# Performance work log

Hardware: AMD Instinct MI355X
Metric: run time of the kernel (lower is better)

The kernel has to match this reference:

```python
import jax, jax.numpy as jnp
import numpy as np

T, S, B, E, H = 1024, 1024, 4, 1024, 16
D = E // H
SCALE = D ** -0.5


def setup_inputs() -> dict:
    key = jax.random.key(0)
    ks = jax.random.split(key, 10)
    std = 0.02
    return {
        "q": jax.random.normal(ks[0], (T, B, E), jnp.float32),
        "k": jax.random.normal(ks[1], (S, B, E), jnp.float32),
        "v": jax.random.normal(ks[2], (S, B, E), jnp.float32),
        "Wq": jax.random.normal(ks[3], (E, E), jnp.float32) * std,
        "Wk": jax.random.normal(ks[4], (E, E), jnp.float32) * std,
        "Wv": jax.random.normal(ks[5], (E, E), jnp.float32) * std,
        "Wp": jax.random.normal(ks[6], (E, E), jnp.float32) * std,
        "bp": jnp.zeros((E,), jnp.float32),
        "attn_bias": jax.random.normal(ks[7], (B, H, T, S), jnp.float32) * std,
        "key_padding_mask": jax.random.bernoulli(ks[8], 0.1, (B, S)),
    }


def reference(q, k, v, Wq, Wk, Wv, Wp, bp, attn_bias, key_padding_mask):
    # projections (no bias: qkv_bias=False); torch Linear is x @ W.T
    qh = (q @ Wq.T).reshape(T, B, H, D).transpose(1, 2, 0, 3) * SCALE  # [B,H,T,D]
    kh = (k @ Wk.T).reshape(S, B, H, D).transpose(1, 2, 0, 3)          # [B,H,S,D]
    vh = (v @ Wv.T).reshape(S, B, H, D).transpose(1, 2, 0, 3)          # [B,H,S,D]

    scores = jnp.einsum("bhid,bhjd->bhij", qh, kh) + attn_bias        # [B,H,T,S]
    # detached max-subtract (as in original)
    scores = scores - jax.lax.stop_gradient(scores.max(axis=-1, keepdims=True))

    mask = key_padding_mask[:, None, None, :]                          # [B,1,1,S], True = masked
    neg = jnp.finfo(scores.dtype).min
    attn = jax.nn.softmax(jnp.where(mask, neg, scores), axis=-1)
    attn = jnp.where(mask, jnp.zeros((), scores.dtype), attn)          # XSoftmax: zero masked probs

    out = jnp.einsum("bhij,bhjd->bhid", attn, vh)                      # [B,H,T,D]
    out = out.transpose(2, 0, 1, 3).reshape(T, B, E)                   # [T,B,E]
    out = out @ Wp.T + bp                                              # output projection
    return (out, attn)
```

## Files before the change

kernel.cpp:

```cpp
#include <hip/hip_runtime.h>
#include <math.h>

constexpr int T_ = 1024, S_ = 1024, B_ = 4, E_ = 1024, H_ = 16, D_ = 64;
constexpr float SCALE_ = 0.125f;
constexpr size_t NH_ = (size_t)B_ * H_ * T_ * D_;
constexpr size_t EE_ = (size_t)E_ * E_;

typedef _Float16 h8 __attribute__((ext_vector_type(8)));
typedef _Float16 h4 __attribute__((ext_vector_type(4)));
typedef float f4 __attribute__((ext_vector_type(4)));

__device__ inline f4 mfma16(h8 a, h8 b, f4 c) {
    return __builtin_amdgcn_mfma_f32_16x16x32_f16(a, b, c, 0, 0, 0);
}

__global__ __launch_bounds__(256) void cvt_all(
    const float* __restrict__ q, const float* __restrict__ k,
    const float* __restrict__ v, const float* __restrict__ wq,
    const float* __restrict__ wk, const float* __restrict__ wv,
    const float* __restrict__ wp, _Float16* __restrict__ dst)
{
    const int i8 = blockIdx.x * 256 + threadIdx.x;
    constexpr int BIG = (int)(NH_ / 8);
    constexpr int WSZ = (int)(EE_ / 8);
    const float* src;
    int loc;
    if (i8 < 3 * BIG) {
        int t = i8 / BIG; loc = i8 - t * BIG;
        src = t == 0 ? q : (t == 1 ? k : v);
    } else {
        int r = i8 - 3 * BIG;
        int t = r / WSZ; loc = r - t * WSZ;
        src = t == 0 ? wq : (t == 1 ? wk : (t == 2 ? wv : wp));
    }
    const float* p = src + (size_t)loc * 8;
    float4 a = *(const float4*)p;
    float4 b = *(const float4*)(p + 4);
    h8 o;
    o[0] = (_Float16)a.x; o[1] = (_Float16)a.y;
    o[2] = (_Float16)a.z; o[3] = (_Float16)a.w;
    o[4] = (_Float16)b.x; o[5] = (_Float16)b.y;
    o[6] = (_Float16)b.z; o[7] = (_Float16)b.w;
    *(h8*)&dst[(size_t)i8 * 8] = o;
}

template <int MODE>
__global__ __launch_bounds__(512) void proj_gemm(
    const _Float16* __restrict__ A, const _Float16* __restrict__ W,
    const float* __restrict__ bias, void* __restrict__ Cv, float scale)
{
    __shared__ _Float16 As[128][72];
    __shared__ _Float16 Bs[128][72];

    const int m0 = blockIdx.x * 128, n0 = blockIdx.y * 128;
    const int tid = threadIdx.x;
    const int w = tid >> 6, l = tid & 63, lr = l & 15, lg = l >> 4;
    const int wr = w >> 2, wc = w & 3;

    f4 acc[4][2];
#pragma unroll
    for (int mi = 0; mi < 4; ++mi)
#pragma unroll
        for (int ni = 0; ni < 2; ++ni) acc[mi][ni] = (f4){0.f, 0.f, 0.f, 0.f};

    for (int k0 = 0; k0 < 1024; k0 += 64) {
#pragma unroll
        for (int i = 0; i < 2; ++i) {
            int f = tid + i * 512;
            int row = f >> 3, c = f & 7;
            *(h8*)&As[row][c * 8] = *(const h8*)&A[(size_t)(m0 + row) * 1024 + k0 + c * 8];
            *(h8*)&Bs[row][c * 8] = *(const h8*)&W[(size_t)(n0 + row) * 1024 + k0 + c * 8];
        }
        __syncthreads();
#pragma unroll
        for (int kk = 0; kk < 2; ++kk) {
            h8 af[4], bf[2];
#pragma unroll
            for (int mi = 0; mi < 4; ++mi)
                af[mi] = *(const h8*)&As[wr * 64 + mi * 16 + lr][kk * 32 + lg * 8];
#pragma unroll
            for (int ni = 0; ni < 2; ++ni)
                bf[ni] = *(const h8*)&Bs[wc * 32 + ni * 16 + lr][kk * 32 + lg * 8];
#pragma unroll
            for (int mi = 0; mi < 4; ++mi)
#pragma unroll
                for (int ni = 0; ni < 2; ++ni)
                    acc[mi][ni] = mfma16(af[mi], bf[ni], acc[mi][ni]);
        }
        __syncthreads();
    }

#pragma unroll
    for (int mi = 0; mi < 4; ++mi)
#pragma unroll
        for (int ni = 0; ni < 2; ++ni)
#pragma unroll
            for (int r = 0; r < 4; ++r) {
                int row = m0 + wr * 64 + mi * 16 + lg * 4 + r;
                int col = n0 + wc * 32 + ni * 16 + lr;
                float vv = acc[mi][ni][r] * scale;
                if (MODE == 0) {
                    int t = row >> 2, b = row & 3, h = col >> 6, d = col & 63;
                    ((_Float16*)Cv)[(((size_t)b * H_ + h) * T_ + t) * D_ + d] = (_Float16)vv;
                } else if (MODE == 1) {
                    int s = row >> 2, b = row & 3, h = col >> 6, d = col & 63;
                    ((_Float16*)Cv)[(((size_t)b * H_ + h) * D_ + d) * S_ + s] = (_Float16)vv;
                } else {
                    ((float*)Cv)[(size_t)row * E_ + col] = vv + bias[col];
                }
            }
}

__global__ __launch_bounds__(512, 6) void fused_attn(
    const _Float16* __restrict__ qh, const _Float16* __restrict__ kh,
    const _Float16* __restrict__ vhT, const float* __restrict__ bias,
    const int* __restrict__ mask, float* __restrict__ attn,
    _Float16* __restrict__ oh)
{
    __shared__ _Float16 Pf[16 * 1024];
    __shared__ int aux_i[1024];
    __shared__ float sinv16[16];
    char* Pb = (char*)Pf;

    const int bid = blockIdx.x;
    const int vid = (bid & 7) * 512 + (bid >> 3);
    const int bh = vid >> 6;
    const int t0 = (vid & 63) * 16;
    const int b = bh >> 4, h = bh & 15;
    const int tid = threadIdx.x;
    const int w = tid >> 6, l = tid & 63, lr = l & 15, lg = l >> 4;

    for (int i = tid; i < S_; i += 512) aux_i[i] = mask[(size_t)b * S_ + i];

    const _Float16* qbase = qh + ((size_t)bh * T_ + t0) * D_;
    h8 qf0 = *(const h8*)&qbase[(size_t)lr * D_ + lg * 8];
    h8 qf1 = *(const h8*)&qbase[(size_t)lr * D_ + 32 + lg * 8];

    const _Float16* kbase = kh + (size_t)bh * S_ * D_;
    const int wbase = w * 128;

    __syncthreads();

#pragma unroll
    for (int sub = 0; sub < 8; ++sub) {
        int s0 = wbase + sub * 16;
        h8 kf0 = *(const h8*)&kbase[(size_t)(s0 + lr) * D_ + lg * 8];
        h8 kf1 = *(const h8*)&kbase[(size_t)(s0 + lr) * D_ + 32 + lg * 8];
        f4 c = (f4){0.f, 0.f, 0.f, 0.f};
        c = mfma16(kf0, qf0, c);
        c = mfma16(kf1, qf1, c);
        int4 mv = *(const int4*)&aux_i[s0 + lg * 4];
        h4 pv;
        pv[0] = mv.x ? (_Float16)0.f : (_Float16)__expf(c[0]);
        pv[1] = mv.y ? (_Float16)0.f : (_Float16)__expf(c[1]);
        pv[2] = mv.z ? (_Float16)0.f : (_Float16)__expf(c[2]);
        pv[3] = mv.w ? (_Float16)0.f : (_Float16)__expf(c[3]);
        int off = (lr * 2048 + (s0 + lg * 4) * 2) ^ ((lr & 7) << 4);
        *(h4*)(Pb + off) = pv;
    }
    __syncthreads();

    {
        const int rr = tid >> 5;
        const int c  = tid & 31;
        const float* brow = bias + ((size_t)bh * T_ + t0 + rr) * S_;

        float4 bv[8];
#pragma unroll
        for (int j = 0; j < 8; ++j)
            bv[j] = *(const float4*)&brow[c * 4 + j * 128];

        h4 p[8];
#pragma unroll
        for (int j = 0; j < 8; ++j) {
            int off = (rr * 2048 + (c * 4 + j * 128) * 2) ^ ((rr & 7) << 4);
            p[j] = *(const h4*)(Pb + off);
        }

        h4 pn[8];
        float rs = 0.f;
#pragma unroll
        for (int j = 0; j < 8; ++j) {
            float p0 = (float)p[j][0] * __expf(bv[j].x);
            float p1 = (float)p[j][1] * __expf(bv[j].y);
            float p2 = (float)p[j][2] * __expf(bv[j].z);
            float p3 = (float)p[j][3] * __expf(bv[j].w);
            rs += (p0 + p1) + (p2 + p3);
            pn[j][0] = (_Float16)p0; pn[j][1] = (_Float16)p1;
            pn[j][2] = (_Float16)p2; pn[j][3] = (_Float16)p3;
        }

        rs += __shfl_xor(rs, 1); rs += __shfl_xor(rs, 2);
        rs += __shfl_xor(rs, 4); rs += __shfl_xor(rs, 8);
        rs += __shfl_xor(rs, 16);
        float inv = 1.0f / rs;
        if (c == 0) sinv16[rr] = inv;

#pragma unroll
        for (int j = 0; j < 8; ++j) {
            int off = (rr * 2048 + (c * 4 + j * 128) * 2) ^ ((rr & 7) << 4);
            *(h4*)(Pb + off) = pn[j];
        }
        float* arow = attn + ((size_t)bh * T_ + t0 + rr) * S_;
#pragma unroll
        for (int j = 0; j < 8; ++j) {
            float4 o = {(float)pn[j][0] * inv, (float)pn[j][1] * inv,
                        (float)pn[j][2] * inv, (float)pn[j][3] * inv};
            *(float4*)&arow[c * 4 + j * 128] = o;
        }
    }
    __syncthreads();

    {
        const int sh = w & 1, dbase = (w >> 1) * 16;
        const _Float16* vbase = vhT + (size_t)bh * D_ * S_;
        f4 acc = (f4){0.f, 0.f, 0.f, 0.f};
#pragma unroll 4
        for (int kc = 0; kc < 16; ++kc) {
            int s0 = sh * 512 + kc * 32;
            int off = (lr * 2048 + (s0 + lg * 8) * 2) ^ ((lr & 7) << 4);
            h8 pf = *(const h8*)(Pb + off);
            h8 vf = *(const h8*)&vbase[(size_t)(dbase + lr) * S_ + s0 + lg * 8];
            acc = mfma16(pf, vf, acc);
        }
        float* pvred = (float*)aux_i;
        if (sh) {
#pragma unroll
            for (int r = 0; r < 4; ++r)
                pvred[(lg * 4 + r) * 64 + dbase + lr] = acc[r];
        }
        __syncthreads();
        if (!sh) {
#pragma unroll
            for (int r = 0; r < 4; ++r) {
                int t = lg * 4 + r;
                float o = (acc[r] + pvred[t * 64 + dbase + lr]) * sinv16[t];
                oh[((size_t)(t0 + t) * B_ + b) * E_ + h * 64 + dbase + lr] = (_Float16)o;
            }
        }
    }
}

extern "C" void kernel_launch(void* const* d_in, const int* in_sizes, int n_in,
                              void* d_out, int out_size, void* d_ws, size_t ws_size,
                              hipStream_t stream)
{
    const float* q    = (const float*)d_in[0];
    const float* k    = (const float*)d_in[1];
    const float* v    = (const float*)d_in[2];
    const float* Wq   = (const float*)d_in[3];
    const float* Wk   = (const float*)d_in[4];
    const float* Wv   = (const float*)d_in[5];
    const float* Wp   = (const float*)d_in[6];
    const float* bp   = (const float*)d_in[7];
    const float* bias = (const float*)d_in[8];
    const int*   mask = (const int*)d_in[9];

    float* out  = (float*)d_out;
    float* attn = out + (size_t)T_ * B_ * E_;

    _Float16* qh   = (_Float16*)d_ws;
    _Float16* kh   = qh + NH_;
    _Float16* vhT  = kh + NH_;
    _Float16* oh   = vhT + NH_;
    _Float16* q16  = oh + NH_;
    _Float16* k16  = q16 + NH_;
    _Float16* v16  = k16 + NH_;
    _Float16* Wq16 = v16 + NH_;
    _Float16* Wk16 = Wq16 + EE_;
    _Float16* Wv16 = Wk16 + EE_;
    _Float16* Wp16 = Wv16 + EE_;

    dim3 blk(512);

    cvt_all<<<dim3(8192), dim3(256), 0, stream>>>(q, k, v, Wq, Wk, Wv, Wp, q16);

    proj_gemm<0><<<dim3(32, 8), blk, 0, stream>>>(q16, Wq16, nullptr, qh, SCALE_);
    proj_gemm<0><<<dim3(32, 8), blk, 0, stream>>>(k16, Wk16, nullptr, kh, 1.0f);
    proj_gemm<1><<<dim3(32, 8), blk, 0, stream>>>(v16, Wv16, nullptr, vhT, 1.0f);

    fused_attn<<<dim3(4096), blk, 0, stream>>>(qh, kh, vhT, bias, mask, attn, oh);

    proj_gemm<2><<<dim3(32, 8), blk, 0, stream>>>(oh, Wp16, bp, out, 1.0f);
}
```

Measured before the change: 299.3 us.

## Merge QKV projections, use direct global-to-LDS loads, smaller tiles, early bias prefetch

The three Q/K/V projection launches become one batched launch using blockIdx.z. The GEMM core changes from 128x128 to 64x128 tiles and stages operands with global_load_lds direct-to-LDS copies into an XOR-swizzled shared layout, which removes the register round trip and the padding. In the attention kernel the attn_bias row is prefetched at kernel start, overlapping it with the QK stage, and the fp32 attention-probability output is written with nontemporal stores. Smaller tiles double the block count and improve GPU fill, at the cost of less reuse per block.

```diff
diff --git a/kernel.cpp b/kernel.cpp
--- a/kernel.cpp
+++ b/kernel.cpp
@@ -12,6 +12,12 @@
 
 __device__ inline f4 mfma16(h8 a, h8 b, f4 c) {
     return __builtin_amdgcn_mfma_f32_16x16x32_f16(a, b, c, 0, 0, 0);
+}
+
+__device__ inline void gload_lds16(const void* g, void* l) {
+    __builtin_amdgcn_global_load_lds(
+        (const __attribute__((address_space(1))) void*)g,
+        (__attribute__((address_space(3))) void*)l, 16, 0, 0);
 }
 
 __global__ __launch_bounds__(256) void cvt_all(
@@ -44,45 +50,52 @@
     *(h8*)&dst[(size_t)i8 * 8] = o;
 }
 
-template <int MODE>
-__global__ __launch_bounds__(512) void proj_gemm(
+template <typename EPI>
+__device__ inline void gemm_core(
     const _Float16* __restrict__ A, const _Float16* __restrict__ W,
-    const float* __restrict__ bias, void* __restrict__ Cv, float scale)
-{
-    __shared__ _Float16 As[128][72];
-    __shared__ _Float16 Bs[128][72];
-
-    const int m0 = blockIdx.x * 128, n0 = blockIdx.y * 128;
+    int m0, int n0, EPI epi)
+{
+    __shared__ _Float16 As[64][64];
+    __shared__ _Float16 Bs[128][64];
+
     const int tid = threadIdx.x;
     const int w = tid >> 6, l = tid & 63, lr = l & 15, lg = l >> 4;
     const int wr = w >> 2, wc = w & 3;
 
-    f4 acc[4][2];
-#pragma unroll
-    for (int mi = 0; mi < 4; ++mi)
+    const int srow = (w << 3) + (l >> 3);
+    const int sg   = (l & 7) ^ (srow & 7);
+    char* AsB = (char*)As;
+    char* BsB = (char*)Bs;
+    char* ldsA  = AsB + w * 1024;
+    char* ldsB0 = BsB + w * 1024;
+    char* ldsB1 = BsB + 8192 + w * 1024;
+
+    f4 acc[2][2];
+#pragma unroll
+    for (int mi = 0; mi < 2; ++mi)
 #pragma unroll
         for (int ni = 0; ni < 2; ++ni) acc[mi][ni] = (f4){0.f, 0.f, 0.f, 0.f};
 
     for (int k0 = 0; k0 < 1024; k0 += 64) {
-#pragma unroll
-        for (int i = 0; i < 2; ++i) {
-            int f = tid + i * 512;
-            int row = f >> 3, c = f & 7;
-            *(h8*)&As[row][c * 8] = *(const h8*)&A[(size_t)(m0 + row) * 1024 + k0 + c * 8];
-            *(h8*)&Bs[row][c * 8] = *(const h8*)&W[(size_t)(n0 + row) * 1024 + k0 + c * 8];
-        }
+        gload_lds16(&A[(size_t)(m0 + srow) * 1024 + k0 + sg * 8], ldsA);
+        gload_lds16(&W[(size_t)(n0 + srow) * 1024 + k0 + sg * 8], ldsB0);
+        gload_lds16(&W[(size_t)(n0 + 64 + srow) * 1024 + k0 + sg * 8], ldsB1);
         __syncthreads();
 #pragma unroll
         for (int kk = 0; kk < 2; ++kk) {
-            h8 af[4], bf[2];
-#pragma unroll
-            for (int mi = 0; mi < 4; ++mi)
-                af[mi] = *(const h8*)&As[wr * 64 + mi * 16 + lr][kk * 32 + lg * 8];
-#pragma unroll
-            for (int ni = 0; ni < 2; ++ni)
-                bf[ni] = *(const h8*)&Bs[wc * 32 + ni * 16 + lr][kk * 32 + lg * 8];
-#pragma unroll
-            for (int mi = 0; mi < 4; ++mi)
+            h8 af[2], bf[2];
+#pragma unroll
+            for (int mi = 0; mi < 2; ++mi) {
+                int r = wr * 32 + mi * 16 + lr, kc = kk * 4 + lg;
+                af[mi] = *(const h8*)(AsB + r * 128 + ((kc ^ (r & 7)) << 4));
+            }
+#pragma unroll
+            for (int ni = 0; ni < 2; ++ni) {
+                int r = wc * 32 + ni * 16 + lr, kc = kk * 4 + lg;
+                bf[ni] = *(const h8*)(BsB + r * 128 + ((kc ^ (r & 7)) << 4));
+            }
+#pragma unroll
+            for (int mi = 0; mi < 2; ++mi)
 #pragma unroll
                 for (int ni = 0; ni < 2; ++ni)
                     acc[mi][ni] = mfma16(af[mi], bf[ni], acc[mi][ni]);
@@ -91,24 +104,52 @@
     }
 
 #pragma unroll
-    for (int mi = 0; mi < 4; ++mi)
+    for (int mi = 0; mi < 2; ++mi)
 #pragma unroll
         for (int ni = 0; ni < 2; ++ni)
 #pragma unroll
             for (int r = 0; r < 4; ++r) {
-                int row = m0 + wr * 64 + mi * 16 + lg * 4 + r;
+                int row = m0 + wr * 32 + mi * 16 + lg * 4 + r;
                 int col = n0 + wc * 32 + ni * 16 + lr;
-                float vv = acc[mi][ni][r] * scale;
-                if (MODE == 0) {
-                    int t = row >> 2, b = row & 3, h = col >> 6, d = col & 63;
-                    ((_Float16*)Cv)[(((size_t)b * H_ + h) * T_ + t) * D_ + d] = (_Float16)vv;
-                } else if (MODE == 1) {
-                    int s = row >> 2, b = row & 3, h = col >> 6, d = col & 63;
-                    ((_Float16*)Cv)[(((size_t)b * H_ + h) * D_ + d) * S_ + s] = (_Float16)vv;
-                } else {
-                    ((float*)Cv)[(size_t)row * E_ + col] = vv + bias[col];
-                }
+                epi(row, col, acc[mi][ni][r]);
             }
+}
+
+__global__ __launch_bounds__(512) void qkv_gemm(
+    const _Float16* __restrict__ q16, const _Float16* __restrict__ k16,
+    const _Float16* __restrict__ v16, const _Float16* __restrict__ Wq16,
+    const _Float16* __restrict__ Wk16, const _Float16* __restrict__ Wv16,
+    _Float16* __restrict__ qh, _Float16* __restrict__ kh,
+    _Float16* __restrict__ vhT)
+{
+    const int z = blockIdx.z;
+    const _Float16* A = z == 0 ? q16 : (z == 1 ? k16 : v16);
+    const _Float16* W = z == 0 ? Wq16 : (z == 1 ? Wk16 : Wv16);
+    _Float16* C = z == 0 ? qh : (z == 1 ? kh : vhT);
+    const float scale = (z == 0) ? SCALE_ : 1.0f;
+    const int m0 = blockIdx.x * 64, n0 = blockIdx.y * 128;
+
+    if (z < 2) {
+        gemm_core(A, W, m0, n0, [&](int row, int col, float vv) {
+            int t = row >> 2, b = row & 3, h = col >> 6, d = col & 63;
+            C[(((size_t)b * H_ + h) * T_ + t) * D_ + d] = (_Float16)(vv * scale);
+        });
+    } else {
+        gemm_core(A, W, m0, n0, [&](int row, int col, float vv) {
+            int s = row >> 2, b = row & 3, h = col >> 6, d = col & 63;
+            C[(((size_t)b * H_ + h) * D_ + d) * S_ + s] = (_Float16)vv;
+        });
+    }
+}
+
+__global__ __launch_bounds__(512) void out_gemm(
+    const _Float16* __restrict__ oh, const _Float16* __restrict__ Wp16,
+    const float* __restrict__ bp, float* __restrict__ out)
+{
+    const int m0 = blockIdx.x * 64, n0 = blockIdx.y * 128;
+    gemm_core(oh, Wp16, m0, n0, [&](int row, int col, float vv) {
+        out[(size_t)row * E_ + col] = vv + bp[col];
+    });
 }
 
 __global__ __launch_bounds__(512, 6) void fused_attn(
@@ -129,6 +170,14 @@
     const int b = bh >> 4, h = bh & 15;
     const int tid = threadIdx.x;
     const int w = tid >> 6, l = tid & 63, lr = l & 15, lg = l >> 4;
+
+    const int rr2 = tid >> 5;
+    const int c2  = tid & 31;
+    const float* brow = bias + ((size_t)bh * T_ + t0 + rr2) * S_;
+    f4 bv[8];
+#pragma unroll
+    for (int j = 0; j < 8; ++j)
+        bv[j] = *(const f4*)&brow[c2 * 4 + j * 128];
 
     for (int i = tid; i < S_; i += 512) aux_i[i] = mask[(size_t)b * S_ + i];
 
@@ -161,19 +210,10 @@
     __syncthreads();
 
     {
-        const int rr = tid >> 5;
-        const int c  = tid & 31;
-        const float* brow = bias + ((size_t)bh * T_ + t0 + rr) * S_;
-
-        float4 bv[8];
-#pragma unroll
-        for (int j = 0; j < 8; ++j)
-            bv[j] = *(const float4*)&brow[c * 4 + j * 128];
-
         h4 p[8];
 #pragma unroll
         for (int j = 0; j < 8; ++j) {
-            int off = (rr * 2048 + (c * 4 + j * 128) * 2) ^ ((rr & 7) << 4);
+            int off = (rr2 * 2048 + (c2 * 4 + j * 128) * 2) ^ ((rr2 & 7) << 4);
             p[j] = *(const h4*)(Pb + off);
         }
 
@@ -181,10 +221,10 @@
         float rs = 0.f;
 #pragma unroll
         for (int j = 0; j < 8; ++j) {
-            float p0 = (float)p[j][0] * __expf(bv[j].x);
-            float p1 = (float)p[j][1] * __expf(bv[j].y);
-            float p2 = (float)p[j][2] * __expf(bv[j].z);
-            float p3 = (float)p[j][3] * __expf(bv[j].w);
+            float p0 = (float)p[j][0] * __expf(bv[j][0]);
+            float p1 = (float)p[j][1] * __expf(bv[j][1]);
+            float p2 = (float)p[j][2] * __expf(bv[j][2]);
+            float p3 = (float)p[j][3] * __expf(bv[j][3]);
             rs += (p0 + p1) + (p2 + p3);
             pn[j][0] = (_Float16)p0; pn[j][1] = (_Float16)p1;
             pn[j][2] = (_Float16)p2; pn[j][3] = (_Float16)p3;
@@ -194,19 +234,19 @@
         rs += __shfl_xor(rs, 4); rs += __shfl_xor(rs, 8);
         rs += __shfl_xor(rs, 16);
         float inv = 1.0f / rs;
-        if (c == 0) sinv16[rr] = inv;
+        if (c2 == 0) sinv16[rr2] = inv;
 
 #pragma unroll
         for (int j = 0; j < 8; ++j) {
-            int off = (rr * 2048 + (c * 4 + j * 128) * 2) ^ ((rr & 7) << 4);
+            int off = (rr2 * 2048 + (c2 * 4 + j * 128) * 2) ^ ((rr2 & 7) << 4);
             *(h4*)(Pb + off) = pn[j];
         }
-        float* arow = attn + ((size_t)bh * T_ + t0 + rr) * S_;
+        float* arow = attn + ((size_t)bh * T_ + t0 + rr2) * S_;
 #pragma unroll
         for (int j = 0; j < 8; ++j) {
-            float4 o = {(float)pn[j][0] * inv, (float)pn[j][1] * inv,
-                        (float)pn[j][2] * inv, (float)pn[j][3] * inv};
-            *(float4*)&arow[c * 4 + j * 128] = o;
+            f4 o = {(float)pn[j][0] * inv, (float)pn[j][1] * inv,
+                    (float)pn[j][2] * inv, (float)pn[j][3] * inv};
+            __builtin_nontemporal_store(o, (f4*)&arow[c2 * 4 + j * 128]);
         }
     }
     __syncthreads();
@@ -275,11 +315,10 @@
 
     cvt_all<<<dim3(8192), dim3(256), 0, stream>>>(q, k, v, Wq, Wk, Wv, Wp, q16);
 
-    proj_gemm<0><<<dim3(32, 8), blk, 0, stream>>>(q16, Wq16, nullptr, qh, SCALE_);
-    proj_gemm<0><<<dim3(32, 8), blk, 0, stream>>>(k16, Wk16, nullptr, kh, 1.0f);
-    proj_gemm<1><<<dim3(32, 8), blk, 0, stream>>>(v16, Wv16, nullptr, vhT, 1.0f);
+    qkv_gemm<<<dim3(64, 8, 3), blk, 0, stream>>>(
+        q16, k16, v16, Wq16, Wk16, Wv16, qh, kh, vhT);
 
     fused_attn<<<dim3(4096), blk, 0, stream>>>(qh, kh, vhT, bias, mask, attn, oh);
 
-    proj_gemm<2><<<dim3(32, 8), blk, 0, stream>>>(oh, Wp16, bp, out, 1.0f);
-}
+    out_gemm<<<dim3(64, 8), blk, 0, stream>>>(oh, Wp16, bp, out);
+}
```

After: 258.2 us. -13.7%, faster.
